# Optimization experiments

Measured on AMD Instinct MI355X. Metric: run time of the kernel, lower is better.

The kernel has to match this reference:

```python
import jax, jax.numpy as jnp
from jax import lax
import numpy as np

T = 64          # psum accumulation length (input elements per partial sum)
NBITS_ACC = 8   # accumulator bit width
Q = 2 ** (NBITS_ACC - 1)  # signed clip range [-Q, Q-1]


def _binarize(x):
    """sign() binarization with straight-through estimator (hardtanh grad)."""
    xc = jnp.clip(x, -1.0, 1.0)
    return xc + lax.stop_gradient(jnp.sign(x) - xc)


def _binconv3x3(x, w, stride=1):
    """Binarized 3x3 conv with digital partial-sum clipping.

    Both activations and weights are binarized to {-1,0,+1} via sign. The
    reduction over Cin*3*3 is split into chunks of T elements; each chunk's
    partial sum is saturated to the nbits_acc-bit signed accumulator range
    before being added to the running total (digital psum scheme).
    """
    xb = _binarize(x)
    wb = _binarize(w)
    O, C, KH, KW = w.shape
    # patches: [N, C*KH*KW, Ho, Wo], feature dim ordered (C, KH, KW)
    patches = lax.conv_general_dilated_patches(
        xb, (KH, KW), (stride, stride), ((1, 1), (1, 1)))
    N, R, Ho, Wo = patches.shape
    G = R // T  # number of psum chunks (2304 / 64 = 36)
    p = patches.reshape(N, G, T, Ho, Wo).transpose(1, 0, 2, 3, 4)  # [G,N,T,H,W]
    wr = wb.reshape(O, G, T).transpose(1, 0, 2)                    # [G,O,T]

    def step(acc, gt):
        pg, wg = gt
        ps = jnp.einsum('nthw,ot->nohw', pg, wg)   # chunk partial sum
        ps = jnp.clip(ps, -float(Q), float(Q - 1))  # accumulator saturation
        return acc + ps, None

    init = jnp.zeros((N, O, Ho, Wo), x.dtype)
    out, _ = lax.scan(step, init, (p, wr))
    return out


def _bn(x, gamma, beta, eps=1e-5):
    # training-mode BatchNorm2d: batch statistics over (N, H, W)
    m = x.mean((0, 2, 3), keepdims=True)
    v = ((x - m) ** 2).mean((0, 2, 3), keepdims=True)
    return (x - m) / jnp.sqrt(v + eps) * gamma[None, :, None, None] + beta[None, :, None, None]


def setup_inputs() -> dict:
    key = jax.random.key(0)
    ks = jax.random.split(key, 3)
    N, C, H, W = 32, 256, 28, 28
    x = jax.random.normal(ks[0], (N, C, H, W), dtype=jnp.float32)
    w1 = jax.random.normal(ks[1], (C, C, 3, 3), dtype=jnp.float32) * 0.05
    w2 = jax.random.normal(ks[2], (C, C, 3, 3), dtype=jnp.float32) * 0.05
    return {
        'x': x,
        'w1': w1,
        'bn1_gamma': jnp.ones((C,), jnp.float32),
        'bn1_beta': jnp.zeros((C,), jnp.float32),
        'w2': w2,
        'bn2_gamma': jnp.ones((C,), jnp.float32),
        'bn2_beta': jnp.zeros((C,), jnp.float32),
    }


def reference(x, w1, bn1_gamma, bn1_beta, w2, bn2_gamma, bn2_beta):
    residual = x
    out = _binconv3x3(x, w1, stride=1)
    out = _bn(out, bn1_gamma, bn1_beta)
    out = jnp.clip(out, -1.0, 1.0)          # Hardtanh
    out = _binconv3x3(out, w2, stride=1)
    out = out + residual                    # identity residual (no downsample)
    out = _bn(out, bn2_gamma, bn2_beta)     # do_bntan=True
    out = jnp.clip(out, -1.0, 1.0)          # Hardtanh
    return out
```

## Files before the change

### kernel.cpp

```cpp
#include <hip/hip_runtime.h>
#include <stdint.h>

typedef unsigned long long u64;

#define NN 32
#define CC 256
#define HH 28
#define WW 28
#define PP 784
#define NHW 25088
#define WPO 36

__global__ __launch_bounds__(256) void pack_x(const float* __restrict__ x, u64* __restrict__ xp) {
    int h = blockIdx.x, n = blockIdx.y;
    int tid = threadIdx.x, lane = tid & 63, g = tid >> 6;
    int c = tid;
    const float* px = x + (((size_t)n * CC + c) * PP) + h * WW;
    float vals[28];
#pragma unroll
    for (int k = 0; k < 7; ++k) ((float4*)vals)[k] = ((const float4*)px)[k];
    u64* dst = xp + ((size_t)n * PP + h * WW) * 4 + g;
#pragma unroll
    for (int i = 0; i < 28; ++i) {
        u64 m = __ballot(vals[i] > 0.0f);
        if (lane == 0) dst[(size_t)i * 4] = m;
    }
}

__global__ __launch_bounds__(256) void pack_wz(const float* __restrict__ w1, const float* __restrict__ w2,
                                               u64* __restrict__ wp1, u64* __restrict__ wp2,
                                               int* s1i, u64* s1q, double* s2s, double* s2q) {
    int o = blockIdx.x, which = blockIdx.y;
    int tid = threadIdx.x, lane = tid & 63, g = tid >> 6;
    if (o == 0 && which == 0) {
        s1i[tid] = 0; s1q[tid] = 0ull; s2s[tid] = 0.0; s2q[tid] = 0.0;
    }
    const float* w = which ? w2 : w1;
    u64* wp = which ? wp2 : wp1;
    const float* pw = w + ((size_t)o * CC + tid) * 9;
#pragma unroll
    for (int tap = 0; tap < 9; ++tap) {
        u64 m = __ballot(pw[tap] > 0.0f);
        if (lane == 0) wp[(size_t)o * WPO + tap * 4 + g] = m;
    }
}


#define POP4(acc, T, WB) \
    acc += __popcll(T[0] ^ wreg[(WB)+0]) + __popcll(T[1] ^ wreg[(WB)+1]) \
         + __popcll(T[2] ^ wreg[(WB)+2]) + __popcll(T[3] ^ wreg[(WB)+3]);

#define LOADROW(T, lrow, ccc) { \
    ulonglong2 u0 = *(const ulonglong2*)&lin[lrow][ccc][0]; \
    ulonglong2 u1 = *(const ulonglong2*)&lin[lrow][ccc][2]; \
    T[0] = u0.x; T[1] = u0.y; T[2] = u1.x; T[3] = u1.y; }

#define COLBODY(ccc, AP, AC, AN) { \
    u64 t0[4], t1[4], t2[4]; \
    LOADROW(t1, wid + 1, ccc) \
    if (rtop) { LOADROW(t0, wid, ccc) } \
    if (rbot) { LOADROW(t2, wid + 2, ccc) } \
    if (rtop) { POP4(AN, t0, 0)  POP4(AC, t0, 4)  POP4(AP, t0, 8)  } \
    POP4(AN, t1, 12) POP4(AC, t1, 16) POP4(AP, t1, 20) \
    if (rbot) { POP4(AN, t2, 24) POP4(AC, t2, 28) POP4(AP, t2, 32) } }

#define EMIT(emc, A) { \
    int K = ((emc) == 0 || (emc) == 27) ? bb2 : bb3; \
    int dot = K - 2 * (A); \
    *vptr = (short)dot; vptr += CC; \
    if (MODE == 0) { tsi += dot; tqi += dot * dot; } \
    else { float u = (float)dot + resrow[emc]; tsf += u; tqf = fmaf(u, u, tqf); } }

template<int MODE>
__global__ __launch_bounds__(256, 3) void binconv(
    const u64* __restrict__ xp, const u64* __restrict__ wp,
    short* __restrict__ vout, const float* __restrict__ xres,
    int* __restrict__ s_i, u64* __restrict__ s_q,
    double* __restrict__ s2s, double* __restrict__ s2q)
{
    __shared__ u64 lin[6][28][4];
    __shared__ double reds[4][64];
    __shared__ double redq[4][64];

    int tid = threadIdx.x, lane = tid & 63, wid = tid >> 6;
    int rt = blockIdx.x, ob = blockIdx.y, n = blockIdx.z;
    int r0 = rt * 4;
    int o = ob * 64 + lane;

    for (int idx = tid; idx < 6 * 56; idx += 256) {
        int row = idx / 56, off = idx % 56;
        int gr = r0 - 1 + row;
        if (gr >= 0 && gr < HH) {
            ulonglong2 t = *(const ulonglong2*)(xp + ((size_t)n * PP + gr * WW) * 4 + off * 2);
            *(ulonglong2*)((u64*)lin + row * 112 + off * 2) = t;
        }
    }

    u64 wreg[36];
    {
        const ulonglong2* wv = (const ulonglong2*)(wp + (size_t)o * WPO);
#pragma unroll
        for (int k = 0; k < 18; ++k) { ulonglong2 t = wv[k]; wreg[2*k] = t.x; wreg[2*k+1] = t.y; }
    }
    __syncthreads();

    int r = r0 + wid;
    const bool rtop = (r > 0), rbot = (r < HH - 1);
    const int nr = 1 + (int)rtop + (int)rbot;
    const int bb3 = 256 * nr * 3, bb2 = 256 * nr * 2;

    short* vptr = vout + ((size_t)n * PP + (size_t)r * WW) * CC + o;
    const float* resrow = (MODE == 1) ? (xres + ((size_t)n * CC + o) * PP + r * WW) : nullptr;

    int tsi = 0, tqi = 0; float tsf = 0.0f, tqf = 0.0f;
    int a = 0, b = 0, c = 0;

    {
        u64 t0[4], t1[4], t2[4];
        LOADROW(t1, wid + 1, 0)
        if (rtop) { LOADROW(t0, wid, 0) }
        if (rbot) { LOADROW(t2, wid + 2, 0) }
        if (rtop) { POP4(c, t0, 0)  POP4(b, t0, 4)  }
        POP4(c, t1, 12) POP4(b, t1, 16)
        if (rbot) { POP4(c, t2, 24) POP4(b, t2, 28) }
    }

#pragma unroll 1
    for (int m = 0; m < 9; ++m) {
        int cc = 3 * m + 1;
        COLBODY(cc,     b, c, a)  EMIT(cc - 1, b)  b = 0;
        COLBODY(cc + 1, c, a, b)  EMIT(cc,     c)  c = 0;
        COLBODY(cc + 2, a, b, c)  EMIT(cc + 1, a)  a = 0;
    }
    EMIT(27, b)

    reds[wid][lane] = (MODE == 0) ? (double)tsi : (double)tsf;
    redq[wid][lane] = (MODE == 0) ? (double)tqi : (double)tqf;
    __syncthreads();
    if (wid == 0) {
        double S = reds[0][lane] + reds[1][lane] + reds[2][lane] + reds[3][lane];
        double Q = redq[0][lane] + redq[1][lane] + redq[2][lane] + redq[3][lane];
        if (MODE == 0) {
            atomicAdd(&s_i[o], (int)S);
            atomicAdd(&s_q[o], (u64)Q);
        } else {
            atomicAdd(&s2s[o], S);
            atomicAdd(&s2q[o], Q);
        }
    }
}

__global__ __launch_bounds__(256) void repack(const short* __restrict__ v1,
                                              const int* __restrict__ s_i, const u64* __restrict__ s_q,
                                              const float* __restrict__ gamma, const float* __restrict__ beta,
                                              u64* __restrict__ xp2) {
    int pt = blockIdx.x, n = blockIdx.y;
    int tid = threadIdx.x, lane = tid & 63, g = tid >> 6;
    int c = tid;
    double mean = (double)s_i[c] * (1.0 / NHW);
    double msq  = (double)s_q[c] * (1.0 / NHW);
    double var  = msq - mean * mean;
    double istd = 1.0 / sqrt(var + 1e-5);
    double ad   = (double)gamma[c] * istd;
    float a = (float)ad;
    float b = (float)((double)beta[c] - mean * ad);
#pragma unroll
    for (int i = 0; i < 16; ++i) {
        int p = pt * 16 + i;
        int v = v1[((size_t)n * PP + p) * CC + c];
        u64 m = __ballot(fmaf(a, (float)v, b) > 0.0f);
        if (lane == 0) xp2[((size_t)n * PP + p) * 4 + g] = m;
    }
}

__global__ __launch_bounds__(256) void finalize(const short* __restrict__ v2, const float* __restrict__ x,
                                                const double* __restrict__ s2s, const double* __restrict__ s2q,
                                                const float* __restrict__ gamma, const float* __restrict__ beta,
                                                float* __restrict__ out) {
    __shared__ short t[64 * 66];
    __shared__ float scs[64], bis[64];
    int ct = blockIdx.x, pt = blockIdx.y, n = blockIdx.z;
    int p0 = pt * 64, c0 = ct * 64;
    int tid = threadIdx.x;
    if (tid < 64) {
        int c = c0 + tid;
        double mean = s2s[c] * (1.0 / NHW);
        double msq  = s2q[c] * (1.0 / NHW);
        double var  = msq - mean * mean;
        double istd = 1.0 / sqrt(var + 1e-5);
        double ad   = (double)gamma[c] * istd;
        scs[tid] = (float)ad;
        bis[tid] = (float)((double)beta[c] - mean * ad);
    }
    for (int idx = tid; idx < 64 * 64; idx += 256) {
        int i = idx >> 6, j = idx & 63;
        int p = p0 + i;
        if (p < PP) t[i * 66 + j] = v2[((size_t)n * PP + p) * CC + c0 + j];
    }
    __syncthreads();
    int pl = tid & 63;
    int p = p0 + pl;
    if (p < PP) {
        for (int cl = tid >> 6; cl < 64; cl += 4) {
            int c = c0 + cl;
            float val = (float)t[pl * 66 + cl] + x[((size_t)n * CC + c) * PP + p];
            float r = fmaf(scs[cl], val, bis[cl]);
            r = fminf(fmaxf(r, -1.0f), 1.0f);
            out[((size_t)n * CC + c) * PP + p] = r;
        }
    }
}

extern "C" void kernel_launch(void* const* d_in, const int* in_sizes, int n_in,
                              void* d_out, int out_size, void* d_ws, size_t ws_size,
                              hipStream_t stream) {
    (void)in_sizes; (void)n_in; (void)out_size; (void)ws_size;
    const float* x   = (const float*)d_in[0];
    const float* w1  = (const float*)d_in[1];
    const float* g1  = (const float*)d_in[2];
    const float* b1  = (const float*)d_in[3];
    const float* w2  = (const float*)d_in[4];
    const float* g2  = (const float*)d_in[5];
    const float* b2  = (const float*)d_in[6];
    float* out = (float*)d_out;

    char* ws = (char*)d_ws;
    u64*    xp1 = (u64*)(ws + 0);
    u64*    xp2 = (u64*)(ws + 802816);
    u64*    wp1 = (u64*)(ws + 1605632);
    u64*    wp2 = (u64*)(ws + 1679360);
    int*    s1i = (int*)(ws + 1753088);
    u64*    s1q = (u64*)(ws + 1754112);
    double* s2s = (double*)(ws + 1756160);
    double* s2q = (double*)(ws + 1758208);
    short*  v12 = (short*)(ws + 1764352);

    pack_wz<<<dim3(256, 2), 256, 0, stream>>>(w1, w2, wp1, wp2, s1i, s1q, s2s, s2q);
    pack_x<<<dim3(28, 32), 256, 0, stream>>>(x, xp1);
    binconv<0><<<dim3(7, 4, 32), 256, 0, stream>>>(xp1, wp1, v12, nullptr, s1i, s1q, nullptr, nullptr);
    repack<<<dim3(49, 32), 256, 0, stream>>>(v12, s1i, s1q, g1, b1, xp2);
    binconv<1><<<dim3(7, 4, 32), 256, 0, stream>>>(xp2, wp2, v12, x, nullptr, nullptr, s2s, s2q);
    finalize<<<dim3(4, 13, 32), 256, 0, stream>>>(v12, x, s2s, s2q, g2, b2, out);
}
```

Measured before the change: 123.9 us.

## Replace XNOR-popcount binary conv with int8 MFMA implicit GEMM

Sign-binarized activations and weights are now stored as int8 ±1 and the 3x3 conv is computed as an implicit GEMM using 32x32x32 i8 MFMA instructions, with swizzled LDS tiles of activations and halo padding. Second-layer BN statistics move into a separate stats2 pass, and scratch buffers for packed inputs and weights are placed in the output buffer. This aims to use matrix cores instead of scalar popcount work. The cost is extra memory traffic from int8 storage, which is 8x larger than bit-packed, plus an additional stats kernel.

```diff
diff --git a/kernel.cpp b/kernel.cpp
--- a/kernel.cpp
+++ b/kernel.cpp
@@ -2,211 +2,233 @@
 #include <stdint.h>
 
 typedef unsigned long long u64;
-
-#define NN 32
-#define CC 256
-#define HH 28
-#define WW 28
-#define PP 784
+typedef int v4i  __attribute__((ext_vector_type(4)));
+typedef int v16i __attribute__((ext_vector_type(16)));
+
+#define PP  784
 #define NHW 25088
-#define WPO 36
-
-__global__ __launch_bounds__(256) void pack_x(const float* __restrict__ x, u64* __restrict__ xp) {
-    int h = blockIdx.x, n = blockIdx.y;
-    int tid = threadIdx.x, lane = tid & 63, g = tid >> 6;
-    int c = tid;
-    const float* px = x + (((size_t)n * CC + c) * PP) + h * WW;
-    float vals[28];
-#pragma unroll
-    for (int k = 0; k < 7; ++k) ((float4*)vals)[k] = ((const float4*)px)[k];
-    u64* dst = xp + ((size_t)n * PP + h * WW) * 4 + g;
-#pragma unroll
-    for (int i = 0; i < 28; ++i) {
-        u64 m = __ballot(vals[i] > 0.0f);
-        if (lane == 0) dst[(size_t)i * 4] = m;
-    }
-}
-
-__global__ __launch_bounds__(256) void pack_wz(const float* __restrict__ w1, const float* __restrict__ w2,
-                                               u64* __restrict__ wp1, u64* __restrict__ wp2,
-                                               int* s1i, u64* s1q, double* s2s, double* s2q) {
-    int o = blockIdx.x, which = blockIdx.y;
-    int tid = threadIdx.x, lane = tid & 63, g = tid >> 6;
-    if (o == 0 && which == 0) {
-        s1i[tid] = 0; s1q[tid] = 0ull; s2s[tid] = 0.0; s2q[tid] = 0.0;
+
+__global__ __launch_bounds__(256) void prepw(const float* __restrict__ w1, const float* __restrict__ w2,
+        signed char* __restrict__ wq1, signed char* __restrict__ wq2,
+        int* s1i, u64* s1q, double* s2s, double* s2q) {
+    int which = blockIdx.x, o = blockIdx.y, cin = threadIdx.x;
+    if (which == 0) {
+        if (o == 0) s1i[cin] = 0;
+        else if (o == 1) s1q[cin] = 0ull;
+        else if (o == 2) s2s[cin] = 0.0;
+        else if (o == 3) s2q[cin] = 0.0;
     }
     const float* w = which ? w2 : w1;
-    u64* wp = which ? wp2 : wp1;
-    const float* pw = w + ((size_t)o * CC + tid) * 9;
-#pragma unroll
-    for (int tap = 0; tap < 9; ++tap) {
-        u64 m = __ballot(pw[tap] > 0.0f);
-        if (lane == 0) wp[(size_t)o * WPO + tap * 4 + g] = m;
-    }
-}
-
-
-#define POP4(acc, T, WB) \
-    acc += __popcll(T[0] ^ wreg[(WB)+0]) + __popcll(T[1] ^ wreg[(WB)+1]) \
-         + __popcll(T[2] ^ wreg[(WB)+2]) + __popcll(T[3] ^ wreg[(WB)+3]);
-
-#define LOADROW(T, lrow, ccc) { \
-    ulonglong2 u0 = *(const ulonglong2*)&lin[lrow][ccc][0]; \
-    ulonglong2 u1 = *(const ulonglong2*)&lin[lrow][ccc][2]; \
-    T[0] = u0.x; T[1] = u0.y; T[2] = u1.x; T[3] = u1.y; }
-
-#define COLBODY(ccc, AP, AC, AN) { \
-    u64 t0[4], t1[4], t2[4]; \
-    LOADROW(t1, wid + 1, ccc) \
-    if (rtop) { LOADROW(t0, wid, ccc) } \
-    if (rbot) { LOADROW(t2, wid + 2, ccc) } \
-    if (rtop) { POP4(AN, t0, 0)  POP4(AC, t0, 4)  POP4(AP, t0, 8)  } \
-    POP4(AN, t1, 12) POP4(AC, t1, 16) POP4(AP, t1, 20) \
-    if (rbot) { POP4(AN, t2, 24) POP4(AC, t2, 28) POP4(AP, t2, 32) } }
-
-#define EMIT(emc, A) { \
-    int K = ((emc) == 0 || (emc) == 27) ? bb2 : bb3; \
-    int dot = K - 2 * (A); \
-    *vptr = (short)dot; vptr += CC; \
-    if (MODE == 0) { tsi += dot; tqi += dot * dot; } \
-    else { float u = (float)dot + resrow[emc]; tsf += u; tqf = fmaf(u, u, tqf); } }
-
-template<int MODE>
-__global__ __launch_bounds__(256, 3) void binconv(
-    const u64* __restrict__ xp, const u64* __restrict__ wp,
-    short* __restrict__ vout, const float* __restrict__ xres,
-    int* __restrict__ s_i, u64* __restrict__ s_q,
-    double* __restrict__ s2s, double* __restrict__ s2q)
-{
-    __shared__ u64 lin[6][28][4];
-    __shared__ double reds[4][64];
-    __shared__ double redq[4][64];
-
+    signed char* wq = which ? wq2 : wq1;
+    int kc = cin >> 5, kh = (cin >> 4) & 1, bx = cin & 15;
+    size_t base = (size_t)kc * 1024 + (size_t)kh * 512 + (size_t)(o & 31) * 16 + bx;
+    int ob = o >> 5;
+#pragma unroll
+    for (int t = 0; t < 9; ++t) {
+        float val = w[((size_t)o * 256 + cin) * 9 + t];
+        wq[(size_t)(t * 8 + ob) * 8192 + base] = (val > 0.0f) ? (signed char)1 : (signed char)-1;
+    }
+}
+
+__global__ __launch_bounds__(256) void prepx(const float* __restrict__ x, signed char* __restrict__ xq) {
+    __shared__ __align__(16) int tT[64 * 68];
+    int pt = blockIdx.x, n = blockIdx.y;
+    int tid = threadIdx.x, lane = tid & 63, wv = tid >> 6;
+    int p0 = pt * 64;
+    int p = p0 + lane, pc = p < PP ? p : (PP - 1);
+#pragma unroll 1
+    for (int pp = 0; pp < 16; ++pp) {
+        int cb = pp * 16 + wv * 4;
+        unsigned word = 0;
+#pragma unroll
+        for (int j = 0; j < 4; ++j) {
+            float val = x[((size_t)n * 256 + cb + j) * PP + pc];
+            unsigned byte = (val > 0.0f) ? 0x01u : 0xFFu;
+            word |= byte << (8 * j);
+        }
+        tT[lane * 68 + pp * 4 + wv] = (int)word;
+    }
+    __syncthreads();
+#pragma unroll 1
+    for (int pass = 0; pass < 4; ++pass) {
+        int s = tid & 15, pq = tid >> 4;
+        int pl = pass * 16 + pq;
+        int pg = p0 + pl;
+        if (pg < PP) {
+            v4i w = *(const v4i*)&tT[pl * 68 + s * 4];
+            *(v4i*)(xq + ((size_t)n * PP + pg) * 256 + s * 16) = w;
+        }
+    }
+}
+
+template<int STATS>
+__global__ __launch_bounds__(256) void mconv(const signed char* __restrict__ xq,
+        const signed char* __restrict__ wq, short* __restrict__ v,
+        int* __restrict__ s1i, u64* __restrict__ s1q) {
+    __shared__ __align__(16) signed char lin[52240];
     int tid = threadIdx.x, lane = tid & 63, wid = tid >> 6;
-    int rt = blockIdx.x, ob = blockIdx.y, n = blockIdx.z;
-    int r0 = rt * 4;
-    int o = ob * 64 + lane;
-
-    for (int idx = tid; idx < 6 * 56; idx += 256) {
-        int row = idx / 56, off = idx % 56;
-        int gr = r0 - 1 + row;
-        if (gr >= 0 && gr < HH) {
-            ulonglong2 t = *(const ulonglong2*)(xp + ((size_t)n * PP + gr * WW) * 4 + off * 2);
-            *(ulonglong2*)((u64*)lin + row * 112 + off * 2) = t;
-        }
-    }
-
-    u64 wreg[36];
+    int kh = lane >> 5, l31 = lane & 31;
+    int p0 = blockIdx.x * 128, nbase = blockIdx.y * 64;
+    int ps0 = p0 - 32;
+
+    for (int idx = tid; idx < 3072; idx += 256) {
+        int fpl = idx >> 4, s = idx & 15;
+        int fp = ps0 + fpl;
+        fp = fp < 0 ? 0 : (fp > NHW - 1 ? NHW - 1 : fp);
+        v4i w = *(const v4i*)(xq + (size_t)fp * 256 + s * 16);
+        *(v4i*)(lin + fpl * 272 + ((s ^ (fpl & 15)) << 4)) = w;
+    }
+    if (tid < 4) ((int*)(lin + 52224))[tid] = 0;
+    __syncthreads();
+
+    int p = p0 + wid * 32 + l31;
+    int pm = p % PP;
+    int r = pm / 28, c = pm - r * 28;
+    int psl = p - ps0;
+    int nb2 = nbase >> 5;
+    v16i acc0 = {}; v16i acc1 = {};
+
+#pragma unroll 1
+    for (int t = 0; t < 9; ++t) {
+        int dr = t / 3, dc = t - dr * 3;
+        bool ok = ((unsigned)(c + dc - 1) < 28u) && ((unsigned)(r + dr - 1) < 28u);
+        int pslT = psl + (dr - 1) * 28 + (dc - 1);
+        int abase = pslT * 272, m15 = pslT & 15;
+        const signed char* wb0 = wq + (size_t)(t * 8 + nb2) * 8192 + (size_t)kh * 512 + (size_t)l31 * 16;
+        const signed char* wb1 = wb0 + 8192;
+#pragma unroll
+        for (int kc = 0; kc < 8; ++kc) {
+            int aoff = ok ? (abase + ((((kc * 2 + kh) ^ m15)) << 4)) : 52224;
+            v4i a  = *(const v4i*)(lin + aoff);
+            v4i b0 = *(const v4i*)(wb0 + kc * 1024);
+            v4i b1 = *(const v4i*)(wb1 + kc * 1024);
+            acc0 = __builtin_amdgcn_mfma_i32_32x32x32_i8(a, b0, acc0, 0, 0, 0);
+            acc1 = __builtin_amdgcn_mfma_i32_32x32x32_i8(a, b1, acc1, 0, 0, 0);
+        }
+    }
+
     {
-        const ulonglong2* wv = (const ulonglong2*)(wp + (size_t)o * WPO);
-#pragma unroll
-        for (int k = 0; k < 18; ++k) { ulonglong2 t = wv[k]; wreg[2*k] = t.x; wreg[2*k+1] = t.y; }
-    }
-    __syncthreads();
-
-    int r = r0 + wid;
-    const bool rtop = (r > 0), rbot = (r < HH - 1);
-    const int nr = 1 + (int)rtop + (int)rbot;
-    const int bb3 = 256 * nr * 3, bb2 = 256 * nr * 2;
-
-    short* vptr = vout + ((size_t)n * PP + (size_t)r * WW) * CC + o;
-    const float* resrow = (MODE == 1) ? (xres + ((size_t)n * CC + o) * PP + r * WW) : nullptr;
-
-    int tsi = 0, tqi = 0; float tsf = 0.0f, tqf = 0.0f;
-    int a = 0, b = 0, c = 0;
-
+        size_t prow = (size_t)(p0 + wid * 32);
+        int ch0 = nbase + l31;
+#pragma unroll
+        for (int j = 0; j < 16; ++j) {
+            int row = (j & 3) + 8 * (j >> 2) + 4 * kh;
+            size_t off = (prow + row) * 256;
+            v[off + ch0]      = (short)acc0[j];
+            v[off + ch0 + 32] = (short)acc1[j];
+        }
+    }
+    if (STATS) {
+        int ss0 = 0, qq0 = 0, ss1 = 0, qq1 = 0;
+#pragma unroll
+        for (int j = 0; j < 16; ++j) {
+            ss0 += acc0[j]; qq0 += acc0[j] * acc0[j];
+            ss1 += acc1[j]; qq1 += acc1[j] * acc1[j];
+        }
+        ss0 += __shfl_xor(ss0, 32); qq0 += __shfl_xor(qq0, 32);
+        ss1 += __shfl_xor(ss1, 32); qq1 += __shfl_xor(qq1, 32);
+        if (lane < 32) {
+            atomicAdd(&s1i[nbase + lane], ss0);
+            atomicAdd(&s1q[nbase + lane], (u64)(unsigned)qq0);
+            atomicAdd(&s1i[nbase + 32 + lane], ss1);
+            atomicAdd(&s1q[nbase + 32 + lane], (u64)(unsigned)qq1);
+        }
+    }
+}
+
+__global__ __launch_bounds__(256) void repack(const short* __restrict__ v,
+        const int* __restrict__ s1i, const u64* __restrict__ s1q,
+        const float* __restrict__ gamma, const float* __restrict__ beta,
+        signed char* __restrict__ xq) {
+    __shared__ float ash[256], bsh[256];
+    int tid = threadIdx.x;
     {
-        u64 t0[4], t1[4], t2[4];
-        LOADROW(t1, wid + 1, 0)
-        if (rtop) { LOADROW(t0, wid, 0) }
-        if (rbot) { LOADROW(t2, wid + 2, 0) }
-        if (rtop) { POP4(c, t0, 0)  POP4(b, t0, 4)  }
-        POP4(c, t1, 12) POP4(b, t1, 16)
-        if (rbot) { POP4(c, t2, 24) POP4(b, t2, 28) }
-    }
-
-#pragma unroll 1
-    for (int m = 0; m < 9; ++m) {
-        int cc = 3 * m + 1;
-        COLBODY(cc,     b, c, a)  EMIT(cc - 1, b)  b = 0;
-        COLBODY(cc + 1, c, a, b)  EMIT(cc,     c)  c = 0;
-        COLBODY(cc + 2, a, b, c)  EMIT(cc + 1, a)  a = 0;
-    }
-    EMIT(27, b)
-
-    reds[wid][lane] = (MODE == 0) ? (double)tsi : (double)tsf;
-    redq[wid][lane] = (MODE == 0) ? (double)tqi : (double)tqf;
-    __syncthreads();
-    if (wid == 0) {
-        double S = reds[0][lane] + reds[1][lane] + reds[2][lane] + reds[3][lane];
-        double Q = redq[0][lane] + redq[1][lane] + redq[2][lane] + redq[3][lane];
-        if (MODE == 0) {
-            atomicAdd(&s_i[o], (int)S);
-            atomicAdd(&s_q[o], (u64)Q);
-        } else {
-            atomicAdd(&s2s[o], S);
-            atomicAdd(&s2q[o], Q);
-        }
-    }
-}
-
-__global__ __launch_bounds__(256) void repack(const short* __restrict__ v1,
-                                              const int* __restrict__ s_i, const u64* __restrict__ s_q,
-                                              const float* __restrict__ gamma, const float* __restrict__ beta,
-                                              u64* __restrict__ xp2) {
-    int pt = blockIdx.x, n = blockIdx.y;
-    int tid = threadIdx.x, lane = tid & 63, g = tid >> 6;
-    int c = tid;
-    double mean = (double)s_i[c] * (1.0 / NHW);
-    double msq  = (double)s_q[c] * (1.0 / NHW);
-    double var  = msq - mean * mean;
-    double istd = 1.0 / sqrt(var + 1e-5);
-    double ad   = (double)gamma[c] * istd;
-    float a = (float)ad;
-    float b = (float)((double)beta[c] - mean * ad);
-#pragma unroll
-    for (int i = 0; i < 16; ++i) {
-        int p = pt * 16 + i;
-        int v = v1[((size_t)n * PP + p) * CC + c];
-        u64 m = __ballot(fmaf(a, (float)v, b) > 0.0f);
-        if (lane == 0) xp2[((size_t)n * PP + p) * 4 + g] = m;
-    }
-}
-
-__global__ __launch_bounds__(256) void finalize(const short* __restrict__ v2, const float* __restrict__ x,
-                                                const double* __restrict__ s2s, const double* __restrict__ s2q,
-                                                const float* __restrict__ gamma, const float* __restrict__ beta,
-                                                float* __restrict__ out) {
+        double mean = (double)s1i[tid] * (1.0 / NHW);
+        double msq  = (double)s1q[tid] * (1.0 / NHW);
+        double var  = msq - mean * mean;
+        double istd = 1.0 / sqrt(var + 1e-5);
+        double ad   = (double)gamma[tid] * istd;
+        ash[tid] = (float)ad;
+        bsh[tid] = (float)((double)beta[tid] - mean * ad);
+    }
+    __syncthreads();
+    int n = blockIdx.y;
+    int p = blockIdx.x * 8 + (tid >> 5), s8 = tid & 31;
+    size_t base = ((size_t)n * PP + p) * 256 + s8 * 8;
+    ulonglong2 raw = *(const ulonglong2*)(v + base);
+    const short* sp = (const short*)&raw;
+    u64 outb = 0;
+#pragma unroll
+    for (int j = 0; j < 8; ++j) {
+        int cc = s8 * 8 + j;
+        float y = fmaf(ash[cc], (float)sp[j], bsh[cc]);
+        u64 byte = (y > 0.0f) ? 0x01ull : 0xFFull;
+        outb |= byte << (8 * j);
+    }
+    *(u64*)(xq + base) = outb;
+}
+
+__global__ __launch_bounds__(256) void stats2(const short* __restrict__ v, const float* __restrict__ x,
+        double* __restrict__ s2s, double* __restrict__ s2q) {
+    __shared__ short t[64 * 66];
+    int pt = blockIdx.x, n = blockIdx.y, tid = threadIdx.x;
+    int p0 = pt * 64;
+    int pl = tid & 63, wv = tid >> 6;
+    int p = p0 + pl; bool okp = p < PP;
+#pragma unroll 1
+    for (int ct = 0; ct < 4; ++ct) {
+        for (int idx = tid; idx < 4096; idx += 256) {
+            int i = idx >> 6, cl = idx & 63;
+            int pi = p0 + i;
+            t[i * 66 + cl] = (pi < PP) ? v[((size_t)n * PP + pi) * 256 + ct * 64 + cl] : (short)0;
+        }
+        __syncthreads();
+#pragma unroll 1
+        for (int cq = 0; cq < 16; ++cq) {
+            int cl = cq * 4 + wv;
+            int cch = ct * 64 + cl;
+            float u = okp ? ((float)t[pl * 66 + cl] + x[((size_t)n * 256 + cch) * PP + p]) : 0.0f;
+            double sd = (double)u, qd = (double)u * (double)u;
+            for (int d = 32; d; d >>= 1) { sd += __shfl_down(sd, d); qd += __shfl_down(qd, d); }
+            if (pl == 0) { atomicAdd(&s2s[cch], sd); atomicAdd(&s2q[cch], qd); }
+        }
+        __syncthreads();
+    }
+}
+
+__global__ __launch_bounds__(256) void finalize(const short* __restrict__ v, const float* __restrict__ x,
+        const double* __restrict__ s2s, const double* __restrict__ s2q,
+        const float* __restrict__ gamma, const float* __restrict__ beta,
+        float* __restrict__ out) {
     __shared__ short t[64 * 66];
     __shared__ float scs[64], bis[64];
-    int ct = blockIdx.x, pt = blockIdx.y, n = blockIdx.z;
-    int p0 = pt * 64, c0 = ct * 64;
-    int tid = threadIdx.x;
+    int ct = blockIdx.x, pt = blockIdx.y, n = blockIdx.z, tid = threadIdx.x;
+    int c0 = ct * 64, p0 = pt * 64;
     if (tid < 64) {
-        int c = c0 + tid;
-        double mean = s2s[c] * (1.0 / NHW);
-        double msq  = s2q[c] * (1.0 / NHW);
+        int cch = c0 + tid;
+        double mean = s2s[cch] * (1.0 / NHW);
+        double msq  = s2q[cch] * (1.0 / NHW);
         double var  = msq - mean * mean;
         double istd = 1.0 / sqrt(var + 1e-5);
-        double ad   = (double)gamma[c] * istd;
+        double ad   = (double)gamma[cch] * istd;
         scs[tid] = (float)ad;
-        bis[tid] = (float)((double)beta[c] - mean * ad);
-    }
-    for (int idx = tid; idx < 64 * 64; idx += 256) {
-        int i = idx >> 6, j = idx & 63;
-        int p = p0 + i;
-        if (p < PP) t[i * 66 + j] = v2[((size_t)n * PP + p) * CC + c0 + j];
+        bis[tid] = (float)((double)beta[cch] - mean * ad);
+    }
+    for (int idx = tid; idx < 4096; idx += 256) {
+        int i = idx >> 6, cl = idx & 63;
+        int pi = p0 + i;
+        t[i * 66 + cl] = (pi < PP) ? v[((size_t)n * PP + pi) * 256 + c0 + cl] : (short)0;
     }
     __syncthreads();
     int pl = tid & 63;
     int p = p0 + pl;
     if (p < PP) {
         for (int cl = tid >> 6; cl < 64; cl += 4) {
-            int c = c0 + cl;
-            float val = (float)t[pl * 66 + cl] + x[((size_t)n * CC + c) * PP + p];
-            float r = fmaf(scs[cl], val, bis[cl]);
-            r = fminf(fmaxf(r, -1.0f), 1.0f);
-            out[((size_t)n * CC + c) * PP + p] = r;
+            int cch = c0 + cl;
+            float val = (float)t[pl * 66 + cl] + x[((size_t)n * 256 + cch) * PP + p];
+            float rr = fmaf(scs[cl], val, bis[cl]);
+            rr = fminf(fmaxf(rr, -1.0f), 1.0f);
+            out[((size_t)n * 256 + cch) * PP + p] = rr;
         }
     }
 }
@@ -224,21 +246,21 @@
     const float* b2  = (const float*)d_in[6];
     float* out = (float*)d_out;
 
+    signed char* xq  = (signed char*)d_out;
+    signed char* wq1 = (signed char*)d_out + 6422528;
+    signed char* wq2 = (signed char*)d_out + 7012352;
     char* ws = (char*)d_ws;
-    u64*    xp1 = (u64*)(ws + 0);
-    u64*    xp2 = (u64*)(ws + 802816);
-    u64*    wp1 = (u64*)(ws + 1605632);
-    u64*    wp2 = (u64*)(ws + 1679360);
-    int*    s1i = (int*)(ws + 1753088);
-    u64*    s1q = (u64*)(ws + 1754112);
-    double* s2s = (double*)(ws + 1756160);
-    double* s2q = (double*)(ws + 1758208);
-    short*  v12 = (short*)(ws + 1764352);
-
-    pack_wz<<<dim3(256, 2), 256, 0, stream>>>(w1, w2, wp1, wp2, s1i, s1q, s2s, s2q);
-    pack_x<<<dim3(28, 32), 256, 0, stream>>>(x, xp1);
-    binconv<0><<<dim3(7, 4, 32), 256, 0, stream>>>(xp1, wp1, v12, nullptr, s1i, s1q, nullptr, nullptr);
-    repack<<<dim3(49, 32), 256, 0, stream>>>(v12, s1i, s1q, g1, b1, xp2);
-    binconv<1><<<dim3(7, 4, 32), 256, 0, stream>>>(xp2, wp2, v12, x, nullptr, nullptr, s2s, s2q);
-    finalize<<<dim3(4, 13, 32), 256, 0, stream>>>(v12, x, s2s, s2q, g2, b2, out);
-}
+    short*  v   = (short*)ws;
+    int*    s1i = (int*)(ws + 12845056);
+    u64*    s1q = (u64*)(ws + 12846080);
+    double* s2s = (double*)(ws + 12848128);
+    double* s2q = (double*)(ws + 12850176);
+
+    prepw<<<dim3(2, 256), 256, 0, stream>>>(w1, w2, wq1, wq2, s1i, s1q, s2s, s2q);
+    prepx<<<dim3(13, 32), 256, 0, stream>>>(x, xq);
+    mconv<1><<<dim3(196, 4), 256, 0, stream>>>(xq, wq1, v, s1i, s1q);
+    repack<<<dim3(98, 32), 256, 0, stream>>>(v, s1i, s1q, g1, b1, xq);
+    mconv<0><<<dim3(196, 4), 256, 0, stream>>>(xq, wq2, v, s1i, s1q);
+    stats2<<<dim3(13, 32), 256, 0, stream>>>(v, x, s2s, s2q);
+    finalize<<<dim3(4, 13, 32), 256, 0, stream>>>(v, x, s2s, s2q, g2, b2, out);
+}
```

Measured after the change: 342.3 us. 176% more time.
